# Kernel optimization log

Measured on AMD Instinct MI355X. Metric: run time of the kernel, lower is better.

## Reference

```python
import jax, jax.numpy as jnp
import numpy as np

D_MODEL = 1024
NUM_HEADS = 16
D_K = D_MODEL // NUM_HEADS
B, S = 2, 2048


def setup_inputs() -> dict:
    key = jax.random.key(0)
    ks = jax.random.split(key, 6)
    scale = 1.0 / np.sqrt(D_MODEL)
    x = jax.random.normal(ks[0], (B, S, D_MODEL), dtype=jnp.float32)
    # causal mask: 1 where masked (future positions), per masked_fill(mask == 1, -inf)
    mask = jnp.triu(jnp.ones((S, S), dtype=jnp.int32), k=1)
    Wq = jax.random.normal(ks[1], (D_MODEL, D_MODEL), dtype=jnp.float32) * scale
    Wk = jax.random.normal(ks[2], (D_MODEL, D_MODEL), dtype=jnp.float32) * scale
    Wv = jax.random.normal(ks[3], (D_MODEL, D_MODEL), dtype=jnp.float32) * scale
    Wo = jax.random.normal(ks[4], (D_MODEL, D_MODEL), dtype=jnp.float32) * scale
    zeros = jnp.zeros((D_MODEL,), dtype=jnp.float32)
    return {"x": x, "mask": mask, "Wq": Wq, "bq": zeros, "Wk": Wk, "bk": zeros,
            "Wv": Wv, "bv": zeros, "Wo": Wo, "bo": zeros}


def reference(x, mask, Wq, bq, Wk, bk, Wv, bv, Wo, bo):
    b, s, d = x.shape
    # linear projections (torch nn.Linear: x @ W^T + b; here W stored as [in, out])
    Q = x @ Wq + bq
    K = x @ Wk + bk
    V = x @ Wv + bv
    # split heads -> (b, h, s, d_k)
    def split(t):
        return t.reshape(b, s, NUM_HEADS, D_K).transpose(0, 2, 1, 3)
    Q, K, V = split(Q), split(K), split(V)
    scale = 1.0 / jnp.sqrt(jnp.float32(D_K))
    scores = jnp.einsum("bhqd,bhkd->bhqk", Q, K) * scale  # (b,h,s,s)
    scores = jnp.where(mask[None, None, :, :] == 1, -jnp.inf, scores)
    attn = jax.nn.softmax(scores, axis=-1)
    out = jnp.einsum("bhqk,bhkd->bhqd", attn, V)
    out = out.transpose(0, 2, 1, 3).reshape(b, s, d)  # concat heads
    return out @ Wo + bo
```

## Files before the change

### kernel.cpp

```cpp
#include <hip/hip_runtime.h>
#include <hip/hip_bf16.h>
#include <cstdint>
#include <cmath>

#define DM 1024
#define NH 16
#define DK 64
#define NB 2
#define SS 2048
#define MM (NB*SS)

typedef unsigned short u16;
typedef uint32_t u32;
typedef __attribute__((ext_vector_type(4))) float f32x4;
typedef __attribute__((ext_vector_type(8))) short s16x8;
typedef __attribute__((ext_vector_type(2))) uint32_t u32x2;

__device__ __forceinline__ u16 f2bf(float f) {
    __hip_bfloat16 h = __float2bfloat16(f);
    return __builtin_bit_cast(u16, h);
}
__device__ __forceinline__ float bf2f(u16 u) {
    u32 x = (u32)u << 16;
    return __builtin_bit_cast(float, x);
}

__device__ __forceinline__ u32 cvtpk(float a, float b) {
    u32 r;
    asm("v_cvt_pk_bf16_f32 %0, %1, %2" : "=v"(r) : "v"(a), "v"(b));
    return r;
}

__device__ __forceinline__ void gload_lds16(void* lds, const void* g) {
    __builtin_amdgcn_global_load_lds(
        (const __attribute__((address_space(1))) uint32_t*)g,
        (__attribute__((address_space(3))) uint32_t*)lds, 16, 0, 0);
}

__device__ __forceinline__ int swz(int row, int cb) {
    return row * 128 + ((((cb) >> 4) ^ (row & 7)) << 4) + ((cb) & 15);
}

#define FENCE_BAR  do { __builtin_amdgcn_sched_barrier(0); \
                        __builtin_amdgcn_s_barrier();      \
                        __builtin_amdgcn_sched_barrier(0); } while (0)

__global__ void mha_prep(const float* __restrict__ x, u16* __restrict__ xb,
                         const float* __restrict__ W0, const float* __restrict__ W1,
                         const float* __restrict__ W2, const float* __restrict__ W3,
                         u16* __restrict__ WtBase) {
    const int bid = blockIdx.x, tid = threadIdx.x;
    if (bid < 4096) {
        int i = (bid * 256 + tid) * 4;
        float4 v = *reinterpret_cast<const float4*>(x + i);
        ushort4 o;
        o.x = f2bf(v.x); o.y = f2bf(v.y); o.z = f2bf(v.z); o.w = f2bf(v.w);
        *reinterpret_cast<ushort4*>(xb + i) = o;
        return;
    }
    __shared__ float t[32][33];
    const int b2 = bid - 4096;
    const int mat = b2 >> 10, rem = b2 & 1023;
    const int cx = rem & 31, cy = rem >> 5;
    const float* W = (mat == 0) ? W0 : (mat == 1) ? W1 : (mat == 2) ? W2 : W3;
    u16* Wt = WtBase + (size_t)mat * DM * DM;
    const int c0 = cx * 32, r0 = cy * 32;
    const int tx = tid & 31, ty = tid >> 5;
#pragma unroll
    for (int i = ty; i < 32; i += 8)
        t[i][tx] = W[(size_t)(r0 + i) * DM + c0 + tx];
    __syncthreads();
#pragma unroll
    for (int i = ty; i < 32; i += 8)
        Wt[(size_t)(c0 + i) * DM + r0 + tx] = f2bf(t[tx][i]);
}

__global__ __launch_bounds__(256, 2) void mha_gemm_qkv(const u16* __restrict__ xb, const u16* __restrict__ Wt,
                                                       const float* __restrict__ bq, const float* __restrict__ bk,
                                                       const float* __restrict__ bv, u16* __restrict__ qkv) {
    __shared__ __align__(16) char smem[81920];

    const int bid = blockIdx.x;
    const int bx = bid & 31, by = bid >> 5;
    const int m0 = bx * 128, n0g = by * 192;

    const int tid = threadIdx.x;
    const int wave = tid >> 6, lane = tid & 63;
    const int lr = lane & 15, kg = lane >> 4;
    const int wr = wave >> 1, wc = wave & 1;

    auto STAGE = [&](int buf, int kt) {
#pragma unroll
        for (int i = 0; i < 4; ++i) {
            const int o = tid * 16 + i * 4096;
            const int r = o >> 7, slot = (o >> 4) & 7;
            gload_lds16(smem + buf * 16384 + o,
                        xb + (size_t)(m0 + r) * DM + kt * 64 + ((slot ^ (r & 7)) << 3));
        }
#pragma unroll
        for (int i = 0; i < 6; ++i) {
            const int o = tid * 16 + i * 4096;
            const int r = o >> 7, slot = (o >> 4) & 7;
            gload_lds16(smem + 32768 + buf * 24576 + o,
                        Wt + (size_t)(n0g + r) * DM + kt * 64 + ((slot ^ (r & 7)) << 3));
        }
    };

    f32x4 acc[4][6] = {};
    STAGE(0, 0);
    for (int t = 0; t < 16; ++t) {
        if (t + 1 < 16) {
            STAGE((t + 1) & 1, t + 1);
            asm volatile("s_waitcnt vmcnt(10)" ::: "memory");
        } else {
            asm volatile("s_waitcnt vmcnt(0)" ::: "memory");
        }
        FENCE_BAR;
        const char* Ab = smem + (t & 1) * 16384;
        const char* Bb = smem + 32768 + (t & 1) * 24576;
#pragma unroll
        for (int ks = 0; ks < 2; ++ks) {
            s16x8 a[4], b[6];
#pragma unroll
            for (int m = 0; m < 4; ++m)
                a[m] = *reinterpret_cast<const s16x8*>(Ab + swz(wr * 64 + m * 16 + lr, ks * 64 + kg * 16));
#pragma unroll
            for (int n = 0; n < 6; ++n)
                b[n] = *reinterpret_cast<const s16x8*>(Bb + swz(wc * 96 + n * 16 + lr, ks * 64 + kg * 16));
#pragma unroll
            for (int m = 0; m < 4; ++m)
#pragma unroll
                for (int n = 0; n < 6; ++n)
                    acc[m][n] = __builtin_amdgcn_mfma_f32_16x16x32_bf16(a[m], b[n], acc[m][n], 0, 0, 0);
        }
        FENCE_BAR;
    }

#pragma unroll
    for (int m = 0; m < 4; ++m)
#pragma unroll
        for (int n = 0; n < 6; ++n) {
            const int colg = n0g + wc * 96 + n * 16 + lr;
            const int z = colg >> 10, coll = colg & 1023;
            const int h = coll >> 6, d = coll & 63;
            const float bv2 = ((z == 0) ? bq : (z == 1) ? bk : bv)[coll];
            const float scale = (z == 0) ? 0.125f * 1.44269504088896f : 1.0f;
            u16* Cout = qkv + (size_t)z * MM * DM;
#pragma unroll
            for (int j = 0; j < 4; ++j) {
                const int row = m0 + wr * 64 + m * 16 + kg * 4 + j;
                const int bb = row >> 11, s = row & (SS - 1);
                const float v = (acc[m][n][j] + bv2) * scale;
                if (z == 0) {
                    Cout[(((size_t)(bb * NH + h) * SS + s) * DK) + d] = f2bf(v);
                } else {
                    const int kt = s >> 6, r = s & 63;
                    const size_t tb = ((size_t)(bb * NH + h) * 32 + kt) * 4096;
                    const int bo = (z == 1) ? swz(r, d * 2)
                                            : swz(d, (r >> 1) * 4 + (r & 1) * 2);
                    Cout[tb + (bo >> 1)] = f2bf(v);
                }
            }
        }
}

__global__ __launch_bounds__(256, 2) void mha_gemm_out(const u16* __restrict__ AO, const u16* __restrict__ WoT,
                                                       const float* __restrict__ bo, float* __restrict__ out) {
    __shared__ __align__(16) char smem[49152];

    const int bid = blockIdx.x;
    const int bx = bid & 31, by = bid >> 5;
    const int m0 = bx * 128, n0 = by * 64;

    const int tid = threadIdx.x;
    const int wave = tid >> 6, lane = tid & 63;
    const int lr = lane & 15, kg = lane >> 4;
    const int wr = wave >> 1, wc = wave & 1;

    auto STAGE = [&](int buf, int kt) {
#pragma unroll
        for (int i = 0; i < 4; ++i) {
            const int o = tid * 16 + i * 4096;
            const int r = o >> 7, slot = (o >> 4) & 7;
            gload_lds16(smem + buf * 16384 + o,
                        AO + (size_t)(m0 + r) * DM + kt * 64 + ((slot ^ (r & 7)) << 3));
        }
#pragma unroll
        for (int i = 0; i < 2; ++i) {
            const int o = tid * 16 + i * 4096;
            const int r = o >> 7, slot = (o >> 4) & 7;
            gload_lds16(smem + 32768 + buf * 8192 + o,
                        WoT + (size_t)(n0 + r) * DM + kt * 64 + ((slot ^ (r & 7)) << 3));
        }
    };

    f32x4 acc[4][2] = {};
    STAGE(0, 0);
    for (int t = 0; t < 16; ++t) {
        if (t + 1 < 16) {
            STAGE((t + 1) & 1, t + 1);
            asm volatile("s_waitcnt vmcnt(6)" ::: "memory");
        } else {
            asm volatile("s_waitcnt vmcnt(0)" ::: "memory");
        }
        FENCE_BAR;
        const char* Ab = smem + (t & 1) * 16384;
        const char* Bb = smem + 32768 + (t & 1) * 8192;
#pragma unroll
        for (int ks = 0; ks < 2; ++ks) {
            s16x8 a[4], b[2];
#pragma unroll
            for (int m = 0; m < 4; ++m)
                a[m] = *reinterpret_cast<const s16x8*>(Ab + swz(wr * 64 + m * 16 + lr, ks * 64 + kg * 16));
#pragma unroll
            for (int n = 0; n < 2; ++n)
                b[n] = *reinterpret_cast<const s16x8*>(Bb + swz(wc * 32 + n * 16 + lr, ks * 64 + kg * 16));
#pragma unroll
            for (int m = 0; m < 4; ++m)
#pragma unroll
                for (int n = 0; n < 2; ++n)
                    acc[m][n] = __builtin_amdgcn_mfma_f32_16x16x32_bf16(a[m], b[n], acc[m][n], 0, 0, 0);
        }
        FENCE_BAR;
    }

#pragma unroll
    for (int m = 0; m < 4; ++m)
#pragma unroll
        for (int n = 0; n < 2; ++n) {
            const int col = n0 + wc * 32 + n * 16 + lr;
            const float bv = bo[col];
#pragma unroll
            for (int j = 0; j < 4; ++j) {
                const int row = m0 + wr * 64 + m * 16 + kg * 4 + j;
                out[(size_t)row * DM + col] = acc[m][n][j] + bv;
            }
        }
}

__device__ const unsigned char JQT[24] = {
    7,15,15, 14,14, 6,13,13, 12,12, 5,11,11, 10,10, 4,9,9, 8,8, 3,2,1,0};
__device__ const unsigned char JKS[24] = {
    0,0,16, 0,15, 0,0,14, 0,13, 0,0,12, 0,11, 0,0,10, 0,9, 0,0,0,0};
__device__ const unsigned char JKL[24] = {
    16,16,16, 15,15, 14,14,14, 13,13, 12,12,12, 11,11, 10,10,10, 9,9, 8,6,4,2};
__device__ const unsigned char JSL[24] = {
    255,14,15, 12,13, 255,10,11, 8,9, 255,6,7, 4,5, 255,2,3, 0,1, 255,255,255,255};

__global__ __launch_bounds__(512, 4) void mha_attn(const u16* __restrict__ Qb, const u16* __restrict__ Kswz,
                                                   const u16* __restrict__ Vtswz, u16* __restrict__ AO,
                                                   u16* __restrict__ Opart, float* __restrict__ lpart) {
    __shared__ __align__(16) char lds[49152];

    const int bid = blockIdx.x;
    const int bh  = bid & 31;
    const int job = bid >> 5;
    const int qt   = JQT[job];
    const int kst  = JKS[job];
    const int klen = JKL[job];
    const int slot = JSL[job];
    const int qb = qt * 128;

    const int tid = threadIdx.x, w = tid >> 6, lane = tid & 63;
    const int lr = lane & 15, kg = lane >> 4;

    const u16* Qh = Qb + (size_t)bh * SS * DK;
    const char* Ktiles = (const char*)(Kswz  + (size_t)bh * 32 * 4096);
    const char* Vtiles = (const char*)(Vtswz + (size_t)bh * 32 * 4096);
    const int bb = bh >> 4, hh = bh & (NH - 1);
    char* psb = lds + 32768 + w * 2048;
    const int o = tid * 16;

    const int qrow = qb + w * 16 + lr;
    const s16x8 qf0 = *reinterpret_cast<const s16x8*>(Qh + (size_t)qrow * DK + kg * 8);
    const s16x8 qf1 = *reinterpret_cast<const s16x8*>(Qh + (size_t)qrow * DK + 32 + kg * 8);
    f32x4 accO[4] = {};
    float lp = 0.f;

    const int kend = kst + klen;
    gload_lds16(lds + o,         Ktiles + kst * 8192 + o);
    gload_lds16(lds + 16384 + o, Vtiles + kst * 8192 + o);

    for (int t = kst; t < kend; ++t) {
        const int buf = (t - kst) & 1;
        asm volatile("s_waitcnt vmcnt(0)" ::: "memory");
        __syncthreads();
        if (t + 1 < kend) {
            gload_lds16(lds + (buf ^ 1) * 8192 + o,         Ktiles + (t + 1) * 8192 + o);
            gload_lds16(lds + 16384 + (buf ^ 1) * 8192 + o, Vtiles + (t + 1) * 8192 + o);
        }
        const char* ksb = lds + buf * 8192;
        const char* vtb = lds + 16384 + buf * 8192;
        const int kb = t * 64;

        f32x4 sc[4];
#pragma unroll
        for (int f = 0; f < 4; ++f) {
            s16x8 kf0 = *reinterpret_cast<const s16x8*>(ksb + swz(f * 16 + lr, kg * 16));
            s16x8 kf1 = *reinterpret_cast<const s16x8*>(ksb + swz(f * 16 + lr, 64 + kg * 16));
            f32x4 s = {};
            s = __builtin_amdgcn_mfma_f32_16x16x32_bf16(kf0, qf0, s, 0, 0, 0);
            s = __builtin_amdgcn_mfma_f32_16x16x32_bf16(kf1, qf1, s, 0, 0, 0);
            sc[f] = s;
        }
#pragma unroll
        for (int f = 0; f < 4; ++f)
#pragma unroll
            for (int j = 0; j < 4; ++j)
                sc[f][j] = __builtin_amdgcn_exp2f(sc[f][j]);
        if (kb + 63 > qb + w * 16) {
            const int qg = qb + w * 16 + lr;
#pragma unroll
            for (int f = 0; f < 4; ++f) {
                const int kc = kb + f * 16 + kg * 4;
#pragma unroll
                for (int j = 0; j < 4; ++j)
                    if (kc + j > qg) sc[f][j] = 0.f;
            }
        }
        float fs0 = 0.f, fs1 = 0.f;
#pragma unroll
        for (int f = 0; f < 4; ++f) {
            u32x2 pp;
            pp[0] = cvtpk(sc[f][0], sc[f][1]);
            pp[1] = cvtpk(sc[f][2], sc[f][3]);
            *reinterpret_cast<u32x2*>(psb + swz(lr, f * 32 + kg * 8)) = pp;
            const float s01 = sc[f][0] + sc[f][1], s23 = sc[f][2] + sc[f][3];
            if (f & 1) fs1 += s01 + s23; else fs0 += s01 + s23;
        }
        lp += fs0 + fs1;

        const s16x8 pf0 = *reinterpret_cast<const s16x8*>(psb + swz(lr, kg * 16));
        const s16x8 pf1 = *reinterpret_cast<const s16x8*>(psb + swz(lr, 64 + kg * 16));
#pragma unroll
        for (int db = 0; db < 4; ++db) {
            s16x8 vf0 = *reinterpret_cast<const s16x8*>(vtb + swz(db * 16 + lr, kg * 16));
            s16x8 vf1 = *reinterpret_cast<const s16x8*>(vtb + swz(db * 16 + lr, 64 + kg * 16));
            accO[db] = __builtin_amdgcn_mfma_f32_16x16x32_bf16(pf0, vf0, accO[db], 0, 0, 0);
            accO[db] = __builtin_amdgcn_mfma_f32_16x16x32_bf16(pf1, vf1, accO[db], 0, 0, 0);
        }
    }

    lp += __shfl_xor(lp, 16, 64);
    lp += __shfl_xor(lp, 32, 64);

    if (slot == 255) {
        float inv[4];
#pragma unroll
        for (int j = 0; j < 4; ++j)
            inv[j] = 1.0f / __shfl(lp, kg * 4 + j, 64);
#pragma unroll
        for (int db = 0; db < 4; ++db) {
            const int d = db * 16 + lr;
#pragma unroll
            for (int j = 0; j < 4; ++j) {
                const int s = qb + w * 16 + kg * 4 + j;
                AO[((size_t)(bb * SS + s)) * DM + hh * DK + d] = f2bf(accO[db][j] * inv[j]);
            }
        }
    } else {
        const int idx = bh * 16 + slot;
        u16* Od = Opart + (size_t)idx * 8192;
#pragma unroll
        for (int db = 0; db < 4; ++db) {
            const int d = db * 16 + lr;
#pragma unroll
            for (int j = 0; j < 4; ++j)
                Od[(w * 16 + kg * 4 + j) * 64 + d] = f2bf(accO[db][j]);
        }
        if (lane < 16)
            lpart[idx * 128 + w * 16 + lane] = lp;
    }
}

__global__ __launch_bounds__(256) void mha_combine(const u16* __restrict__ Opart,
                                                   const float* __restrict__ lpart,
                                                   u16* __restrict__ AO) {
    const int blk = blockIdx.x;
    const int bh = blk & 31, q = blk >> 5;
    const int qt = 8 + q;
    const int t = threadIdx.x;
    const int row = t >> 1, c0 = (t & 1) * 32;
    const int idx0 = bh * 16 + q * 2;
    const u16* O0 = Opart + (size_t)idx0 * 8192 + row * 64 + c0;
    const u16* O1 = O0 + 8192;
    const float l = lpart[idx0 * 128 + row] + lpart[(idx0 + 1) * 128 + row];
    const float inv = 1.0f / l;
    const int bb = bh >> 4, hh = bh & (NH - 1);
    const int s = qt * 128 + row;
    u16* dst = AO + ((size_t)(bb * SS + s)) * DM + hh * DK + c0;
#pragma unroll
    for (int h = 0; h < 4; ++h) {
        s16x8 a = *reinterpret_cast<const s16x8*>(O0 + h * 8);
        s16x8 b = *reinterpret_cast<const s16x8*>(O1 + h * 8);
        u16* ap = (u16*)&a; u16* bp = (u16*)&b;
        u16 ov[8];
#pragma unroll
        for (int i = 0; i < 8; ++i)
            ov[i] = f2bf((bf2f(ap[i]) + bf2f(bp[i])) * inv);
        *reinterpret_cast<ushort4*>(dst + h * 8) = *reinterpret_cast<ushort4*>(&ov[0]);
        *reinterpret_cast<ushort4*>(dst + h * 8 + 4) = *reinterpret_cast<ushort4*>(&ov[4]);
    }
}

extern "C" void kernel_launch(void* const* d_in, const int* in_sizes, int n_in,
                              void* d_out, int out_size, void* d_ws, size_t ws_size,
                              hipStream_t stream) {
    const float* x  = (const float*)d_in[0];
    const float* Wq = (const float*)d_in[2];
    const float* bq = (const float*)d_in[3];
    const float* Wk = (const float*)d_in[4];
    const float* bk = (const float*)d_in[5];
    const float* Wv = (const float*)d_in[6];
    const float* bv = (const float*)d_in[7];
    const float* Wo = (const float*)d_in[8];
    const float* bo = (const float*)d_in[9];
    float* out = (float*)d_out;

    char* ws = (char*)d_ws;
    u16* xb  = (u16*)(ws);
    u16* Wt  = (u16*)(ws + ((size_t)8  << 20));
    u16* qkv = (u16*)(ws + ((size_t)16 << 20));
    u16* AO  = (u16*)(ws + ((size_t)40 << 20));
    u16*   Opart = (u16*)(ws);
    float* lpart = (float*)(ws + ((size_t)8 << 20));

    mha_prep<<<dim3(8192), dim3(256), 0, stream>>>(x, xb, Wq, Wk, Wv, Wo, Wt);
    mha_gemm_qkv<<<dim3(512), dim3(256), 0, stream>>>(xb, Wt, bq, bk, bv, qkv);
    mha_attn<<<dim3(768), dim3(512), 0, stream>>>(qkv, qkv + (size_t)4194304, qkv + (size_t)8388608,
                                                  AO, Opart, lpart);
    mha_combine<<<dim3(256), dim3(256), 0, stream>>>(Opart, lpart, AO);
    mha_gemm_out<<<dim3(512), dim3(256), 0, stream>>>(AO, Wt + (size_t)3 * DM * DM, bo, out);
}
```

Before: 98.31 us.

## Drop split-KV attention scheduling and combine kernel; one block per query tile

Replaces the job-table split-KV schedule, where long causal query tiles were split in two with partial outputs merged by a separate combine kernel, with one block per full query tile ordered longest-first. This removes the partial-output writes, the combine launch and its extra global traffic. In exchange, load balance is worse: the longest blocks now process twice as many key tiles, which can lengthen the critical path when all blocks are resident at once.

```diff
diff --git a/kernel.cpp b/kernel.cpp
--- a/kernel.cpp
+++ b/kernel.cpp
@@ -19,10 +19,6 @@
 __device__ __forceinline__ u16 f2bf(float f) {
     __hip_bfloat16 h = __float2bfloat16(f);
     return __builtin_bit_cast(u16, h);
-}
-__device__ __forceinline__ float bf2f(u16 u) {
-    u32 x = (u32)u << 16;
-    return __builtin_bit_cast(float, x);
 }
 
 __device__ __forceinline__ u32 cvtpk(float a, float b) {
@@ -238,28 +234,17 @@
         }
 }
 
-__device__ const unsigned char JQT[24] = {
-    7,15,15, 14,14, 6,13,13, 12,12, 5,11,11, 10,10, 4,9,9, 8,8, 3,2,1,0};
-__device__ const unsigned char JKS[24] = {
-    0,0,16, 0,15, 0,0,14, 0,13, 0,0,12, 0,11, 0,0,10, 0,9, 0,0,0,0};
-__device__ const unsigned char JKL[24] = {
-    16,16,16, 15,15, 14,14,14, 13,13, 12,12,12, 11,11, 10,10,10, 9,9, 8,6,4,2};
-__device__ const unsigned char JSL[24] = {
-    255,14,15, 12,13, 255,10,11, 8,9, 255,6,7, 4,5, 255,2,3, 0,1, 255,255,255,255};
+__device__ const unsigned char PERM[16] = {15,14,13,12,11,10,9,8, 0,1,2,3,4,5,6,7};
 
 __global__ __launch_bounds__(512, 4) void mha_attn(const u16* __restrict__ Qb, const u16* __restrict__ Kswz,
-                                                   const u16* __restrict__ Vtswz, u16* __restrict__ AO,
-                                                   u16* __restrict__ Opart, float* __restrict__ lpart) {
+                                                   const u16* __restrict__ Vtswz, u16* __restrict__ AO) {
     __shared__ __align__(16) char lds[49152];
 
     const int bid = blockIdx.x;
     const int bh  = bid & 31;
-    const int job = bid >> 5;
-    const int qt   = JQT[job];
-    const int kst  = JKS[job];
-    const int klen = JKL[job];
-    const int slot = JSL[job];
-    const int qb = qt * 128;
+    const int qt  = PERM[bid >> 5];
+    const int qb  = qt * 128;
+    const int nkt = 2 * qt + 2;
 
     const int tid = threadIdx.x, w = tid >> 6, lane = tid & 63;
     const int lr = lane & 15, kg = lane >> 4;
@@ -277,15 +262,14 @@
     f32x4 accO[4] = {};
     float lp = 0.f;
 
-    const int kend = kst + klen;
-    gload_lds16(lds + o,         Ktiles + kst * 8192 + o);
-    gload_lds16(lds + 16384 + o, Vtiles + kst * 8192 + o);
-
-    for (int t = kst; t < kend; ++t) {
-        const int buf = (t - kst) & 1;
+    gload_lds16(lds + o,         Ktiles + o);
+    gload_lds16(lds + 16384 + o, Vtiles + o);
+
+    for (int t = 0; t < nkt; ++t) {
+        const int buf = t & 1;
         asm volatile("s_waitcnt vmcnt(0)" ::: "memory");
         __syncthreads();
-        if (t + 1 < kend) {
+        if (t + 1 < nkt) {
             gload_lds16(lds + (buf ^ 1) * 8192 + o,         Ktiles + (t + 1) * 8192 + o);
             gload_lds16(lds + 16384 + (buf ^ 1) * 8192 + o, Vtiles + (t + 1) * 8192 + o);
         }
@@ -344,62 +328,18 @@
     lp += __shfl_xor(lp, 16, 64);
     lp += __shfl_xor(lp, 32, 64);
 
-    if (slot == 255) {
-        float inv[4];
-#pragma unroll
-        for (int j = 0; j < 4; ++j)
-            inv[j] = 1.0f / __shfl(lp, kg * 4 + j, 64);
-#pragma unroll
-        for (int db = 0; db < 4; ++db) {
-            const int d = db * 16 + lr;
-#pragma unroll
-            for (int j = 0; j < 4; ++j) {
-                const int s = qb + w * 16 + kg * 4 + j;
-                AO[((size_t)(bb * SS + s)) * DM + hh * DK + d] = f2bf(accO[db][j] * inv[j]);
-            }
-        }
-    } else {
-        const int idx = bh * 16 + slot;
-        u16* Od = Opart + (size_t)idx * 8192;
-#pragma unroll
-        for (int db = 0; db < 4; ++db) {
-            const int d = db * 16 + lr;
-#pragma unroll
-            for (int j = 0; j < 4; ++j)
-                Od[(w * 16 + kg * 4 + j) * 64 + d] = f2bf(accO[db][j]);
-        }
-        if (lane < 16)
-            lpart[idx * 128 + w * 16 + lane] = lp;
-    }
-}
-
-__global__ __launch_bounds__(256) void mha_combine(const u16* __restrict__ Opart,
-                                                   const float* __restrict__ lpart,
-                                                   u16* __restrict__ AO) {
-    const int blk = blockIdx.x;
-    const int bh = blk & 31, q = blk >> 5;
-    const int qt = 8 + q;
-    const int t = threadIdx.x;
-    const int row = t >> 1, c0 = (t & 1) * 32;
-    const int idx0 = bh * 16 + q * 2;
-    const u16* O0 = Opart + (size_t)idx0 * 8192 + row * 64 + c0;
-    const u16* O1 = O0 + 8192;
-    const float l = lpart[idx0 * 128 + row] + lpart[(idx0 + 1) * 128 + row];
-    const float inv = 1.0f / l;
-    const int bb = bh >> 4, hh = bh & (NH - 1);
-    const int s = qt * 128 + row;
-    u16* dst = AO + ((size_t)(bb * SS + s)) * DM + hh * DK + c0;
-#pragma unroll
-    for (int h = 0; h < 4; ++h) {
-        s16x8 a = *reinterpret_cast<const s16x8*>(O0 + h * 8);
-        s16x8 b = *reinterpret_cast<const s16x8*>(O1 + h * 8);
-        u16* ap = (u16*)&a; u16* bp = (u16*)&b;
-        u16 ov[8];
-#pragma unroll
-        for (int i = 0; i < 8; ++i)
-            ov[i] = f2bf((bf2f(ap[i]) + bf2f(bp[i])) * inv);
-        *reinterpret_cast<ushort4*>(dst + h * 8) = *reinterpret_cast<ushort4*>(&ov[0]);
-        *reinterpret_cast<ushort4*>(dst + h * 8 + 4) = *reinterpret_cast<ushort4*>(&ov[4]);
+    float inv[4];
+#pragma unroll
+    for (int j = 0; j < 4; ++j)
+        inv[j] = 1.0f / __shfl(lp, kg * 4 + j, 64);
+#pragma unroll
+    for (int db = 0; db < 4; ++db) {
+        const int d = db * 16 + lr;
+#pragma unroll
+        for (int j = 0; j < 4; ++j) {
+            const int s = qb + w * 16 + kg * 4 + j;
+            AO[((size_t)(bb * SS + s)) * DM + hh * DK + d] = f2bf(accO[db][j] * inv[j]);
+        }
     }
 }
 
@@ -422,13 +362,9 @@
     u16* Wt  = (u16*)(ws + ((size_t)8  << 20));
     u16* qkv = (u16*)(ws + ((size_t)16 << 20));
     u16* AO  = (u16*)(ws + ((size_t)40 << 20));
-    u16*   Opart = (u16*)(ws);
-    float* lpart = (float*)(ws + ((size_t)8 << 20));
 
     mha_prep<<<dim3(8192), dim3(256), 0, stream>>>(x, xb, Wq, Wk, Wv, Wo, Wt);
     mha_gemm_qkv<<<dim3(512), dim3(256), 0, stream>>>(xb, Wt, bq, bk, bv, qkv);
-    mha_attn<<<dim3(768), dim3(512), 0, stream>>>(qkv, qkv + (size_t)4194304, qkv + (size_t)8388608,
-                                                  AO, Opart, lpart);
-    mha_combine<<<dim3(256), dim3(256), 0, stream>>>(Opart, lpart, AO);
+    mha_attn<<<dim3(512), dim3(512), 0, stream>>>(qkv, qkv + (size_t)4194304, qkv + (size_t)8388608, AO);
     mha_gemm_out<<<dim3(512), dim3(256), 0, stream>>>(AO, Wt + (size_t)3 * DM * DM, bo, out);
 }
```

Result: faster. 95.23 us, median of 2 (-3.1%).
